# Optimization experiments

Measured on AMD Instinct MI355X. Metric: run time of the kernel, lower is better.

## Reference

```python
import jax, jax.numpy as jnp
import numpy as np

D_MODEL = 1024
NUM_HEADS = 16
HEAD_DIM = D_MODEL // NUM_HEADS


def setup_inputs() -> dict:
    key = jax.random.key(0)
    ks = jax.random.split(key, 5)
    B, S, D_IN = 2, 2048, 1024
    x = jax.random.normal(ks[0], (B, S, D_IN), dtype=jnp.float32)
    std = 0.02
    wq = jax.random.normal(ks[1], (D_MODEL, D_IN), dtype=jnp.float32) * std
    wk = jax.random.normal(ks[2], (D_MODEL, D_IN), dtype=jnp.float32) * std
    wv = jax.random.normal(ks[3], (D_MODEL, D_IN), dtype=jnp.float32) * std
    wo = jax.random.normal(ks[4], (D_IN, D_MODEL), dtype=jnp.float32) * std
    return {"x": x, "wq": wq, "wk": wk, "wv": wv, "wo": wo}


def _mha(x, wq, wk, wv, wo):
    B, S, _ = x.shape
    H, Dh = NUM_HEADS, HEAD_DIM
    # projections: Linear applies x @ W.T with W of shape [out, in]
    q = (x @ wq.T).reshape(B, S, H, Dh).transpose(0, 2, 1, 3)  # [B,H,S,Dh]
    k = (x @ wk.T).reshape(B, S, H, Dh).transpose(0, 2, 1, 3)
    v = (x @ wv.T).reshape(B, S, H, Dh).transpose(0, 2, 1, 3)
    scores = jnp.einsum('bhqd,bhkd->bhqk', q, k) / jnp.sqrt(jnp.float32(Dh))
    causal = jnp.tril(jnp.ones((S, S), dtype=bool))  # True where attended
    scores = jnp.where(causal, scores, -jnp.inf)
    attn = jax.nn.softmax(scores, axis=-1)
    out = jnp.einsum('bhqk,bhkd->bhqd', attn, v)  # [B,H,S,Dh]
    out = out.transpose(0, 2, 1, 3).reshape(B, S, H * Dh)
    return out @ wo.T


def reference(x, wq, wk, wv, wo):
    return _mha(x, wq, wk, wv, wo)
```

## Files before the change

kernel.cpp:

```cpp
#include <hip/hip_runtime.h>
#include <hip/hip_bf16.h>
#include <stdint.h>

using bf16 = __hip_bfloat16;
typedef __attribute__((ext_vector_type(4))) short shorts4;
typedef __attribute__((ext_vector_type(8))) short short8;
typedef __attribute__((ext_vector_type(4))) float floatx4;
typedef __attribute__((ext_vector_type(16))) float floatx16;
typedef __attribute__((ext_vector_type(4))) unsigned int uintx4;

constexpr int BATCH = 2;
constexpr int SEQ   = 2048;
constexpr int NH    = 16;
constexpr int DH    = 64;
constexpr int DM    = 1024;
constexpr int MROWS = BATCH * SEQ;
constexpr int OUTN  = MROWS * DM;
constexpr int WN    = DM * DM;

__device__ inline short bfbits(float x) {
    bf16 h = __float2bfloat16(x);
    return __builtin_bit_cast(short, h);
}

__device__ inline unsigned pack2(float a, float b) {
    return (unsigned)(unsigned short)bfbits(a) |
           ((unsigned)(unsigned short)bfbits(b) << 16);
}

__device__ inline void async16(bf16* lds, const bf16* g) {
    __builtin_amdgcn_global_load_lds(
        (const __attribute__((address_space(1))) unsigned int*)g,
        (__attribute__((address_space(3))) unsigned int*)lds, 16, 0, 0);
}

__device__ inline void cvt8(const float* src, bf16* dst) {
    float4 f0 = *(const float4*)(src);
    float4 f1 = *(const float4*)(src + 4);
    short8 o;
    o[0] = bfbits(f0.x); o[1] = bfbits(f0.y); o[2] = bfbits(f0.z); o[3] = bfbits(f0.w);
    o[4] = bfbits(f1.x); o[5] = bfbits(f1.y); o[6] = bfbits(f1.z); o[7] = bfbits(f1.w);
    *(short8*)(dst) = o;
}

__global__ __launch_bounds__(256)
void cvt_all(const float* __restrict__ x,  const float* __restrict__ wq,
             const float* __restrict__ wk, const float* __restrict__ wv,
             const float* __restrict__ wo, bf16* __restrict__ dst,
             bf16* __restrict__ wob)
{
    const size_t i = ((size_t)blockIdx.x * 256 + threadIdx.x) * 8;
    if (i < (size_t)OUTN + 3 * WN) {
        const float* src; size_t off;
        if (i < (size_t)OUTN)               { src = x;  off = i; }
        else if (i < (size_t)OUTN + WN)     { src = wq; off = i - OUTN; }
        else if (i < (size_t)OUTN + 2 * WN) { src = wk; off = i - OUTN - WN; }
        else                                { src = wv; off = i - OUTN - 2 * (size_t)WN; }
        cvt8(src + off, dst + i);
    } else {
        const size_t off = i - OUTN - 3 * (size_t)WN;
        cvt8(wo + off, wob + off);
    }
}

__global__ __launch_bounds__(256)
void cvt_inputs(const float* __restrict__ x,  const float* __restrict__ wq,
                const float* __restrict__ wk, const float* __restrict__ wv,
                bf16* __restrict__ dst)
{
    const size_t i = ((size_t)blockIdx.x * 256 + threadIdx.x) * 8;
    const float* src; size_t off;
    if (i < (size_t)OUTN)               { src = x;  off = i; }
    else if (i < (size_t)OUTN + WN)     { src = wq; off = i - OUTN; }
    else if (i < (size_t)OUTN + 2 * WN) { src = wk; off = i - OUTN - WN; }
    else                                { src = wv; off = i - OUTN - 2 * (size_t)WN; }
    cvt8(src + off, dst + i);
}

__global__ __launch_bounds__(256)
void cvt_wo(const float* __restrict__ wo, bf16* __restrict__ dst)
{
    const size_t i = ((size_t)blockIdx.x * 256 + threadIdx.x) * 8;
    cvt8(wo + i, dst + i);
}

template<int MODE, int NZ>
__global__ __launch_bounds__(512, 2)
void gemm_mfma(const bf16* __restrict__ A,
               const bf16* __restrict__ W0, const bf16* __restrict__ W1,
               const bf16* __restrict__ W2,
               bf16* __restrict__ C0, bf16* __restrict__ C1, bf16* __restrict__ C2,
               float* __restrict__ F)
{
    __shared__ __align__(16) bf16 smem[(1 + NZ) * 8192 * 2];

    const int t    = threadIdx.x;
    const int wave = t >> 6;
    const int lane = t & 63;
    const int quad = lane >> 4;
    const int l16  = lane & 15;
    const int m0 = blockIdx.y * 128;
    const int n0 = blockIdx.x * 128;
    const int wr = (wave >> 2) * 64;
    const int wc = (wave & 3) * 32;

    const bf16* Wp[3] = {W0, W1, W2};

    floatx4 acc[NZ][4][2] = {};

    auto stage = [&](int kt, int bb) {
        bf16* Bb = smem + bb * (1 + NZ) * 8192;
        const int k0 = kt * 64;
        #pragma unroll
        for (int p = 0; p < 2; p++) {
            const int ck = p * 512 + t;
            const int kr = ck >> 3;
            const int kg = (ck & 7) ^ (kr & 7);
            async16(Bb + ck * 8, A + (size_t)(m0 + kr) * DM + k0 + kg * 8);
            #pragma unroll
            for (int zz = 0; zz < NZ; zz++)
                async16(Bb + (1 + zz) * 8192 + ck * 8,
                        Wp[zz] + (size_t)(n0 + kr) * DM + k0 + kg * 8);
        }
    };

    stage(0, 0);
    __syncthreads();

    for (int kt = 0; kt < DM / 64; ++kt) {
        const int cur = kt & 1;
        if (kt + 1 < DM / 64) stage(kt + 1, cur ^ 1);

        const bf16* Bb = smem + cur * (1 + NZ) * 8192;

        #pragma unroll
        for (int ks = 0; ks < 2; ks++) {
            short8 af[4];
            #pragma unroll
            for (int i = 0; i < 4; i++) {
                const int r = wr + i * 16 + l16;
                af[i] = *(const short8*)(Bb + r * 64 + ((ks * 4 + quad) ^ (r & 7)) * 8);
            }
            #pragma unroll
            for (int zz = 0; zz < NZ; zz++) {
                short8 wf[2];
                #pragma unroll
                for (int j = 0; j < 2; j++) {
                    const int n = wc + j * 16 + l16;
                    wf[j] = *(const short8*)(Bb + (1 + zz) * 8192 + n * 64 +
                                             ((ks * 4 + quad) ^ (n & 7)) * 8);
                }
                __builtin_amdgcn_s_setprio(1);
                #pragma unroll
                for (int i = 0; i < 4; i++)
                    #pragma unroll
                    for (int j = 0; j < 2; j++)
                        acc[zz][i][j] = __builtin_amdgcn_mfma_f32_16x16x32_bf16(
                            af[i], wf[j], acc[zz][i][j], 0, 0, 0);
                __builtin_amdgcn_s_setprio(0);
            }
        }
        __syncthreads();
    }

    #pragma unroll
    for (int zz = 0; zz < NZ; zz++) {
        #pragma unroll
        for (int i = 0; i < 4; i++) {
            #pragma unroll
            for (int j = 0; j < 2; j++) {
                if (MODE == 0 && zz == 2) {
                    const int s0 = m0 + wr + i * 16 + quad * 4;
                    const int gn = n0 + wc + j * 16 + l16;
                    const int b = s0 >> 11, sr = s0 & (SEQ - 1);
                    const int h = gn >> 6,  d = gn & (DH - 1);
                    shorts4 pv;
                    #pragma unroll
                    for (int r = 0; r < 4; r++) pv[r] = bfbits(acc[zz][i][j][r]);
                    *(shorts4*)(C2 + (((size_t)(b * NH + h)) * DH + d) * SEQ + sr) = pv;
                } else {
                    #pragma unroll
                    for (int r = 0; r < 4; r++) {
                        const int gm = m0 + wr + i * 16 + quad * 4 + r;
                        const int gn = n0 + wc + j * 16 + l16;
                        if (MODE == 1) {
                            F[(size_t)gm * DM + gn] = acc[zz][i][j][r];
                        } else {
                            float av = acc[zz][i][j][r];
                            if (zz == 0) av *= 0.18033688f;
                            bf16* dst = (zz == 0) ? C0 : C1;
                            dst[(size_t)gm * DM + gn] = __float2bfloat16(av);
                        }
                    }
                }
            }
        }
    }
}

__global__ __launch_bounds__(512, 2)
void attn_flash(bf16* __restrict__ Q, const bf16* __restrict__ K,
                const bf16* __restrict__ Vt)
{
    __shared__ __align__(16) bf16 smem[49152];

    const int t    = threadIdx.x;
    const int wave = t >> 6;
    const int lane = t & 63;
    const int hi   = lane >> 5;
    const int l32  = lane & 31;

    const int h   = blockIdx.y;
    const int b   = blockIdx.z;
    const int qtA = blockIdx.x;
    const int qtB = 15 - qtA;
    const int hc  = h * DH;
    const size_t rowb = (size_t)b * SEQ;
    const size_t bhv  = ((size_t)(b * NH + h)) * SEQ * DH;

    const int qw    = wave & 3;
    const int khalf = wave >> 2;
    const int qrA = qtA * 128 + qw * 32;
    const int qrB = qtB * 128 + qw * 32;

    short8 qfA[4], qfB[4];
    #pragma unroll
    for (int sg = 0; sg < 4; sg++) {
        qfA[sg] = *(const short8*)(Q + (rowb + qrA + l32) * DM + hc + sg * 16 + hi * 8);
        qfB[sg] = *(const short8*)(Q + (rowb + qrB + l32) * DM + hc + sg * 16 + hi * 8);
    }

    floatx16 oaccA[2] = {}, oaccB[2] = {};
    float lsumA = 0.f, lsumB = 0.f;

    constexpr int NSLOT = 17;

    auto slotK0 = [&](int s) { return (s <= qtA ? s : s - qtA - 1) * 128; };

    auto stage = [&](int s) {
        bf16* Kb = smem + (s % 3) * 16384;
        bf16* Vb = Kb + 8192;
        const int k0 = slotK0(s);
        #pragma unroll
        for (int p = 0; p < 2; p++) {
            const int ck = p * 512 + t;
            const int kr = ck >> 3;
            const int kg = (ck & 7) ^ (kr & 7);
            async16(Kb + ck * 8, K + (rowb + k0 + kr) * DM + hc + kg * 8);
            const int vr = ck >> 4;
            const int vg = (ck & 15) ^ (vr & 15);
            async16(Vb + ck * 8, Vt + bhv + (size_t)vr * SEQ + k0 + vg * 8);
        }
    };

    auto computeStage = [&](int s, int k0, int qrow, const short8* qf,
                            floatx16* oacc, float& lsum) {
        const int kbase = k0 + khalf * 64;
        if (kbase > qrow + 31) return;
        const bf16* Ks = smem + (s % 3) * 16384;
        const bf16* Vs = Ks + 8192;
        const int qg = qrow + l32;

        #pragma unroll
        for (int kt = 0; kt < 2; kt++) {
            const int kb = kbase + kt * 32;
            if (kb > qrow + 31) continue;

            const int krow = khalf * 64 + kt * 32 + l32;
            floatx16 sc = {};
            #pragma unroll
            for (int sg = 0; sg < 4; sg++) {
                const int g = (sg * 2 + hi) ^ (krow & 7);
                short8 kf = *(const short8*)(Ks + krow * 64 + g * 8);
                sc = __builtin_amdgcn_mfma_f32_32x32x16_bf16(kf, qf[sg], sc, 0, 0, 0);
            }

            if (kb + 31 > qrow) {
                #pragma unroll
                for (int r = 0; r < 16; r++) {
                    const int key = kb + (r & 3) + 8 * (r >> 2) + 4 * hi;
                    sc[r] = (key <= qg) ? sc[r] : -1e30f;
                }
            }

            #pragma unroll
            for (int r = 0; r < 16; r++) {
                const float p = __builtin_amdgcn_exp2f(sc[r]);
                sc[r] = p;
                lsum += p;
            }

            unsigned d[4][2];
            #pragma unroll
            for (int g = 0; g < 4; g++) {
                d[g][0] = pack2(sc[4 * g + 0], sc[4 * g + 1]);
                d[g][1] = pack2(sc[4 * g + 2], sc[4 * g + 3]);
            }

            #pragma unroll
            for (int h16 = 0; h16 < 2; h16++) {
                const unsigned a0 = d[h16 * 2][0],     a1 = d[h16 * 2][1];
                const unsigned b0 = d[h16 * 2 + 1][0], b1 = d[h16 * 2 + 1][1];
                const unsigned mine0 = hi ? b0 : a0, mine1 = hi ? b1 : a1;
                const unsigned give0 = hi ? a0 : b0, give1 = hi ? a1 : b1;
                const unsigned r0 = (unsigned)__shfl_xor((int)give0, 32, 64);
                const unsigned r1 = (unsigned)__shfl_xor((int)give1, 32, 64);
                uintx4 pw;
                pw[0] = hi ? r0 : mine0;
                pw[1] = hi ? r1 : mine1;
                pw[2] = hi ? mine0 : r0;
                pw[3] = hi ? mine1 : r1;
                short8 pb = __builtin_bit_cast(short8, pw);

                const int Gbase = khalf * 8 + kt * 4 + h16 * 2 + hi;
                #pragma unroll
                for (int tile = 0; tile < 2; tile++) {
                    const int vrow = tile * 32 + l32;
                    const int vg = Gbase ^ (vrow & 15);
                    short8 vf = *(const short8*)(Vs + vrow * 128 + vg * 8);
                    oacc[tile] = __builtin_amdgcn_mfma_f32_32x32x16_bf16(vf, pb, oacc[tile], 0, 0, 0);
                }
            }
        }
    };

    stage(0);
    stage(1);
    for (int s = 0; s < NSLOT - 1; ++s) {
        asm volatile("s_waitcnt vmcnt(4)" ::: "memory");
        __builtin_amdgcn_s_barrier();
        if (s + 2 < NSLOT) stage(s + 2);
        if (s <= qtA) computeStage(s, s * 128, qrA, qfA, oaccA, lsumA);
        else          computeStage(s, (s - qtA - 1) * 128, qrB, qfB, oaccB, lsumB);
    }
    asm volatile("s_waitcnt vmcnt(0)" ::: "memory");
    __builtin_amdgcn_s_barrier();
    computeStage(NSLOT - 1, (NSLOT - 1 - qtA - 1) * 128, qrB, qfB, oaccB, lsumB);

    lsumA += __shfl_xor(lsumA, 32, 64);
    lsumB += __shfl_xor(lsumB, 32, 64);

    __syncthreads();
    float* dmp = (float*)smem;
    float* lP  = dmp + 2 * 4 * 32 * 66;
    if (khalf == 1) {
        #pragma unroll
        for (int m = 0; m < 2; m++) {
            const floatx16* oc = m ? oaccB : oaccA;
            #pragma unroll
            for (int tile = 0; tile < 2; tile++)
                #pragma unroll
                for (int r = 0; r < 16; r++) {
                    const int dd = tile * 32 + (r & 3) + 8 * (r >> 2) + 4 * hi;
                    dmp[((m * 4 + qw) * 32 + l32) * 66 + dd] = oc[tile][r];
                }
            if (!hi) lP[(m * 4 + qw) * 32 + l32] = m ? lsumB : lsumA;
        }
    }
    __syncthreads();

    if (khalf == 0) {
        bf16* T8 = smem + 34304 + qw * 2304;
        #pragma unroll
        for (int m = 0; m < 2; m++) {
            const floatx16* oc = m ? oaccB : oaccA;
            const float lt = (m ? lsumB : lsumA) + lP[(m * 4 + qw) * 32 + l32];
            const float invl = 1.0f / lt;
            const int qrow = m ? qrB : qrA;
            #pragma unroll
            for (int tile = 0; tile < 2; tile++)
                #pragma unroll
                for (int rq = 0; rq < 4; rq++) {
                    shorts4 v4;
                    #pragma unroll
                    for (int sg = 0; sg < 4; sg++) {
                        const int r = rq * 4 + sg;
                        const int dd = tile * 32 + (r & 3) + 8 * (r >> 2) + 4 * hi;
                        const float comb = oc[tile][r] + dmp[((m * 4 + qw) * 32 + l32) * 66 + dd];
                        v4[sg] = bfbits(comb * invl);
                    }
                    *(shorts4*)(T8 + l32 * 72 + tile * 32 + rq * 8 + hi * 4) = v4;
                }
            asm volatile("s_waitcnt lgkmcnt(0)" ::: "memory");
            #pragma unroll
            for (int p2 = 0; p2 < 4; p2++) {
                const int rq = (lane >> 3) + p2 * 8;
                const int dd = (lane & 7) * 8;
                short8 v8 = *(const short8*)(T8 + rq * 72 + dd);
                *(short8*)(Q + (rowb + qrow + rq) * DM + hc + dd) = v8;
            }
            asm volatile("s_waitcnt lgkmcnt(0)" ::: "memory");
        }
    }
}

extern "C" void kernel_launch(void* const* d_in, const int* in_sizes, int n_in,
                              void* d_out, int out_size, void* d_ws, size_t ws_size,
                              hipStream_t stream)
{
    const float* x  = (const float*)d_in[0];
    const float* wq = (const float*)d_in[1];
    const float* wk = (const float*)d_in[2];
    const float* wv = (const float*)d_in[3];
    const float* wo = (const float*)d_in[4];
    float* out = (float*)d_out;

    bf16* qb = (bf16*)d_ws;
    bf16* kb = qb + (size_t)OUTN;
    bf16* vb = kb + (size_t)OUTN;

    bf16* xb  = (bf16*)d_out;
    bf16* wqb = xb + (size_t)OUTN;
    bf16* wkb = wqb + WN;
    bf16* wvb = wkb + WN;

    const bool wsBig = ws_size >= (size_t)(3 * (size_t)OUTN + WN) * sizeof(bf16);

    if (wsBig) {
        bf16* wob = vb + (size_t)OUTN;
        cvt_all<<<(OUTN + 4 * WN) / (8 * 256), 256, 0, stream>>>(
            x, wq, wk, wv, wo, xb, wob);
        gemm_mfma<0, 3><<<dim3(DM / 128, MROWS / 128), dim3(512), 0, stream>>>(
            xb, wqb, wkb, wvb, qb, kb, vb, nullptr);
        attn_flash<<<dim3(8, NH, BATCH), dim3(512), 0, stream>>>(qb, kb, vb);
        gemm_mfma<1, 1><<<dim3(DM / 128, MROWS / 128), dim3(512), 0, stream>>>(
            qb, wob, nullptr, nullptr, nullptr, nullptr, nullptr, out);
    } else {
        cvt_inputs<<<(OUTN + 3 * WN) / (8 * 256), 256, 0, stream>>>(x, wq, wk, wv, xb);
        gemm_mfma<0, 3><<<dim3(DM / 128, MROWS / 128), dim3(512), 0, stream>>>(
            xb, wqb, wkb, wvb, qb, kb, vb, nullptr);
        attn_flash<<<dim3(8, NH, BATCH), dim3(512), 0, stream>>>(qb, kb, vb);
        bf16* wob = kb;
        cvt_wo<<<WN / (8 * 256), 256, 0, stream>>>(wo, wob);
        gemm_mfma<1, 1><<<dim3(DM / 128, MROWS / 128), dim3(512), 0, stream>>>(
            qb, wob, nullptr, nullptr, nullptr, nullptr, nullptr, out);
    }
}
```

Before: 159.1 us.

## Rewrite QKV GEMM with 256x256 tiles, per-projection grid z, and split prefetch

The fused QKV projection, which used 128x128 tiles with all three weights staged per block, becomes a dedicated kernel with 256x256 tiles and one projection per blockIdx.z. Its K loop is split into four MFMA phases, each fenced by barriers and sched_barrier, with the next tile's A and W halves prefetched between phases. The goal is higher arithmetic intensity per LDS byte and better overlap of global loads with MFMA work. The costs are 128 KB of shared memory per block (the launch bound still asks for 2 blocks per CU, which may not fit), more barriers, a larger accumulator register footprint, and fewer blocks in the grid. The output projection and attention body are only refactored into non-templated code.

```diff
diff --git a/kernel.cpp b/kernel.cpp
--- a/kernel.cpp
+++ b/kernel.cpp
@@ -84,15 +84,171 @@
     cvt8(wo + i, dst + i);
 }
 
-template<int MODE, int NZ>
 __global__ __launch_bounds__(512, 2)
-void gemm_mfma(const bf16* __restrict__ A,
-               const bf16* __restrict__ W0, const bf16* __restrict__ W1,
-               const bf16* __restrict__ W2,
-               bf16* __restrict__ C0, bf16* __restrict__ C1, bf16* __restrict__ C2,
+void gemm_qkv(const bf16* __restrict__ A,
+              const bf16* __restrict__ W0, const bf16* __restrict__ W1,
+              const bf16* __restrict__ W2,
+              bf16* __restrict__ C0, bf16* __restrict__ C1, bf16* __restrict__ C2)
+{
+    __shared__ __align__(16) bf16 smem[65536];
+
+    const int t    = threadIdx.x;
+    const int wave = t >> 6;
+    const int lane = t & 63;
+    const int quad = lane >> 4;
+    const int l16  = lane & 15;
+    const int n0 = blockIdx.x * 256;
+    const int m0 = blockIdx.y * 256;
+    const int z  = blockIdx.z;
+    const bf16* W = (z == 0) ? W0 : ((z == 1) ? W1 : W2);
+
+    const int wm = wave >> 2;
+    const int wn = wave & 3;
+
+    floatx4 acc[8][4] = {};
+
+    auto stageHalf = [&](int kt, int bb, int tb, int h) {
+        const bf16* src = tb ? W : A;
+        const int br = tb ? n0 : m0;
+        bf16* dst = smem + bb * 32768 + tb * 16384 + h * 8192;
+        const int k0 = kt * 64;
+        #pragma unroll
+        for (int p = 0; p < 2; p++) {
+            const int ck = p * 512 + t;
+            const int kr = h * 128 + (ck >> 3);
+            const int kc = (ck & 7) ^ (kr & 7);
+            async16(dst + ck * 8, src + (size_t)(br + kr) * DM + k0 + kc * 8);
+        }
+    };
+
+    stageHalf(0, 0, 0, 0); stageHalf(0, 0, 0, 1);
+    stageHalf(0, 0, 1, 0); stageHalf(0, 0, 1, 1);
+    asm volatile("s_waitcnt vmcnt(0)" ::: "memory");
+    __builtin_amdgcn_s_barrier();
+
+    for (int kt = 0; kt < 16; ++kt) {
+        const int cur = kt & 1;
+        const bf16* Ab = smem + cur * 32768;
+        const bf16* Wb = Ab + 16384;
+        const bool pf = (kt + 1 < 16);
+
+        short8 af[4], ag[4], wf[4];
+
+        #pragma unroll
+        for (int i = 0; i < 4; i++) {
+            const int r = wm * 128 + i * 16 + l16;
+            af[i] = *(const short8*)(Ab + r * 64 + (quad ^ (r & 7)) * 8);
+        }
+        #pragma unroll
+        for (int j = 0; j < 4; j++) {
+            const int n = wn * 64 + j * 16 + l16;
+            wf[j] = *(const short8*)(Wb + n * 64 + (quad ^ (n & 7)) * 8);
+        }
+        if (pf) { stageHalf(kt + 1, cur ^ 1, 0, 0); stageHalf(kt + 1, cur ^ 1, 0, 1); }
+        __builtin_amdgcn_s_barrier();
+        asm volatile("s_waitcnt lgkmcnt(0)" ::: "memory");
+        __builtin_amdgcn_sched_barrier(0);
+        __builtin_amdgcn_s_setprio(1);
+        #pragma unroll
+        for (int i = 0; i < 4; i++)
+            #pragma unroll
+            for (int j = 0; j < 4; j++)
+                acc[i][j] = __builtin_amdgcn_mfma_f32_16x16x32_bf16(af[i], wf[j], acc[i][j], 0, 0, 0);
+        __builtin_amdgcn_s_setprio(0);
+        __builtin_amdgcn_s_barrier();
+
+        #pragma unroll
+        for (int i = 0; i < 4; i++) {
+            const int r = wm * 128 + 64 + i * 16 + l16;
+            ag[i] = *(const short8*)(Ab + r * 64 + (quad ^ (r & 7)) * 8);
+        }
+        if (pf) { stageHalf(kt + 1, cur ^ 1, 1, 0); stageHalf(kt + 1, cur ^ 1, 1, 1); }
+        __builtin_amdgcn_s_barrier();
+        asm volatile("s_waitcnt lgkmcnt(0)" ::: "memory");
+        __builtin_amdgcn_sched_barrier(0);
+        __builtin_amdgcn_s_setprio(1);
+        #pragma unroll
+        for (int i = 0; i < 4; i++)
+            #pragma unroll
+            for (int j = 0; j < 4; j++)
+                acc[4 + i][j] = __builtin_amdgcn_mfma_f32_16x16x32_bf16(ag[i], wf[j], acc[4 + i][j], 0, 0, 0);
+        __builtin_amdgcn_s_setprio(0);
+        __builtin_amdgcn_s_barrier();
+
+        #pragma unroll
+        for (int i = 0; i < 4; i++) {
+            const int r = wm * 128 + i * 16 + l16;
+            af[i] = *(const short8*)(Ab + r * 64 + ((4 + quad) ^ (r & 7)) * 8);
+        }
+        #pragma unroll
+        for (int j = 0; j < 4; j++) {
+            const int n = wn * 64 + j * 16 + l16;
+            wf[j] = *(const short8*)(Wb + n * 64 + ((4 + quad) ^ (n & 7)) * 8);
+        }
+        __builtin_amdgcn_s_barrier();
+        asm volatile("s_waitcnt lgkmcnt(0)" ::: "memory");
+        __builtin_amdgcn_sched_barrier(0);
+        __builtin_amdgcn_s_setprio(1);
+        #pragma unroll
+        for (int i = 0; i < 4; i++)
+            #pragma unroll
+            for (int j = 0; j < 4; j++)
+                acc[i][j] = __builtin_amdgcn_mfma_f32_16x16x32_bf16(af[i], wf[j], acc[i][j], 0, 0, 0);
+        __builtin_amdgcn_s_setprio(0);
+        __builtin_amdgcn_s_barrier();
+
+        #pragma unroll
+        for (int i = 0; i < 4; i++) {
+            const int r = wm * 128 + 64 + i * 16 + l16;
+            ag[i] = *(const short8*)(Ab + r * 64 + ((4 + quad) ^ (r & 7)) * 8);
+        }
+        __builtin_amdgcn_s_barrier();
+        asm volatile("s_waitcnt lgkmcnt(0)" ::: "memory");
+        __builtin_amdgcn_sched_barrier(0);
+        __builtin_amdgcn_s_setprio(1);
+        #pragma unroll
+        for (int i = 0; i < 4; i++)
+            #pragma unroll
+            for (int j = 0; j < 4; j++)
+                acc[4 + i][j] = __builtin_amdgcn_mfma_f32_16x16x32_bf16(ag[i], wf[j], acc[4 + i][j], 0, 0, 0);
+        __builtin_amdgcn_s_setprio(0);
+        asm volatile("s_waitcnt vmcnt(0)" ::: "memory");
+        __builtin_amdgcn_s_barrier();
+    }
+
+    #pragma unroll
+    for (int mi = 0; mi < 8; mi++) {
+        #pragma unroll
+        for (int j = 0; j < 4; j++) {
+            if (z == 2) {
+                const int s0 = m0 + wm * 128 + mi * 16 + quad * 4;
+                const int gn = n0 + wn * 64 + j * 16 + l16;
+                const int b = s0 >> 11, sr = s0 & (SEQ - 1);
+                const int h = gn >> 6,  d = gn & (DH - 1);
+                shorts4 pv;
+                #pragma unroll
+                for (int r = 0; r < 4; r++) pv[r] = bfbits(acc[mi][j][r]);
+                *(shorts4*)(C2 + (((size_t)(b * NH + h)) * DH + d) * SEQ + sr) = pv;
+            } else {
+                #pragma unroll
+                for (int r = 0; r < 4; r++) {
+                    const int gm = m0 + wm * 128 + mi * 16 + quad * 4 + r;
+                    const int gn = n0 + wn * 64 + j * 16 + l16;
+                    float av = acc[mi][j][r];
+                    if (z == 0) av *= 0.18033688f;
+                    bf16* dst = (z == 0) ? C0 : C1;
+                    dst[(size_t)gm * DM + gn] = __float2bfloat16(av);
+                }
+            }
+        }
+    }
+}
+
+__global__ __launch_bounds__(512, 2)
+void gemm_proj(const bf16* __restrict__ A, const bf16* __restrict__ W0,
                float* __restrict__ F)
 {
-    __shared__ __align__(16) bf16 smem[(1 + NZ) * 8192 * 2];
+    __shared__ __align__(16) bf16 smem[2 * 8192 * 2];
 
     const int t    = threadIdx.x;
     const int wave = t >> 6;
@@ -104,12 +260,10 @@
     const int wr = (wave >> 2) * 64;
     const int wc = (wave & 3) * 32;
 
-    const bf16* Wp[3] = {W0, W1, W2};
-
-    floatx4 acc[NZ][4][2] = {};
+    floatx4 acc[4][2] = {};
 
     auto stage = [&](int kt, int bb) {
-        bf16* Bb = smem + bb * (1 + NZ) * 8192;
+        bf16* Bb = smem + bb * 16384;
         const int k0 = kt * 64;
         #pragma unroll
         for (int p = 0; p < 2; p++) {
@@ -117,10 +271,7 @@
             const int kr = ck >> 3;
             const int kg = (ck & 7) ^ (kr & 7);
             async16(Bb + ck * 8, A + (size_t)(m0 + kr) * DM + k0 + kg * 8);
-            #pragma unroll
-            for (int zz = 0; zz < NZ; zz++)
-                async16(Bb + (1 + zz) * 8192 + ck * 8,
-                        Wp[zz] + (size_t)(n0 + kr) * DM + k0 + kg * 8);
+            async16(Bb + 8192 + ck * 8, W0 + (size_t)(n0 + kr) * DM + k0 + kg * 8);
         }
     };
 
@@ -131,68 +282,111 @@
         const int cur = kt & 1;
         if (kt + 1 < DM / 64) stage(kt + 1, cur ^ 1);
 
-        const bf16* Bb = smem + cur * (1 + NZ) * 8192;
+        const bf16* Bb = smem + cur * 16384;
 
         #pragma unroll
         for (int ks = 0; ks < 2; ks++) {
-            short8 af[4];
+            short8 af[4], wf[2];
             #pragma unroll
             for (int i = 0; i < 4; i++) {
                 const int r = wr + i * 16 + l16;
                 af[i] = *(const short8*)(Bb + r * 64 + ((ks * 4 + quad) ^ (r & 7)) * 8);
             }
             #pragma unroll
-            for (int zz = 0; zz < NZ; zz++) {
-                short8 wf[2];
+            for (int j = 0; j < 2; j++) {
+                const int n = wc + j * 16 + l16;
+                wf[j] = *(const short8*)(Bb + 8192 + n * 64 + ((ks * 4 + quad) ^ (n & 7)) * 8);
+            }
+            __builtin_amdgcn_s_setprio(1);
+            #pragma unroll
+            for (int i = 0; i < 4; i++)
                 #pragma unroll
-                for (int j = 0; j < 2; j++) {
-                    const int n = wc + j * 16 + l16;
-                    wf[j] = *(const short8*)(Bb + (1 + zz) * 8192 + n * 64 +
-                                             ((ks * 4 + quad) ^ (n & 7)) * 8);
-                }
-                __builtin_amdgcn_s_setprio(1);
-                #pragma unroll
-                for (int i = 0; i < 4; i++)
-                    #pragma unroll
-                    for (int j = 0; j < 2; j++)
-                        acc[zz][i][j] = __builtin_amdgcn_mfma_f32_16x16x32_bf16(
-                            af[i], wf[j], acc[zz][i][j], 0, 0, 0);
-                __builtin_amdgcn_s_setprio(0);
-            }
+                for (int j = 0; j < 2; j++)
+                    acc[i][j] = __builtin_amdgcn_mfma_f32_16x16x32_bf16(af[i], wf[j], acc[i][j], 0, 0, 0);
+            __builtin_amdgcn_s_setprio(0);
         }
         __syncthreads();
     }
 
     #pragma unroll
-    for (int zz = 0; zz < NZ; zz++) {
-        #pragma unroll
-        for (int i = 0; i < 4; i++) {
-            #pragma unroll
-            for (int j = 0; j < 2; j++) {
-                if (MODE == 0 && zz == 2) {
-                    const int s0 = m0 + wr + i * 16 + quad * 4;
-                    const int gn = n0 + wc + j * 16 + l16;
-                    const int b = s0 >> 11, sr = s0 & (SEQ - 1);
-                    const int h = gn >> 6,  d = gn & (DH - 1);
-                    shorts4 pv;
-                    #pragma unroll
-                    for (int r = 0; r < 4; r++) pv[r] = bfbits(acc[zz][i][j][r]);
-                    *(shorts4*)(C2 + (((size_t)(b * NH + h)) * DH + d) * SEQ + sr) = pv;
-                } else {
-                    #pragma unroll
-                    for (int r = 0; r < 4; r++) {
-                        const int gm = m0 + wr + i * 16 + quad * 4 + r;
-                        const int gn = n0 + wc + j * 16 + l16;
-                        if (MODE == 1) {
-                            F[(size_t)gm * DM + gn] = acc[zz][i][j][r];
-                        } else {
-                            float av = acc[zz][i][j][r];
-                            if (zz == 0) av *= 0.18033688f;
-                            bf16* dst = (zz == 0) ? C0 : C1;
-                            dst[(size_t)gm * DM + gn] = __float2bfloat16(av);
-                        }
-                    }
-                }
+    for (int i = 0; i < 4; i++)
+        #pragma unroll
+        for (int j = 0; j < 2; j++)
+            #pragma unroll
+            for (int r = 0; r < 4; r++) {
+                const int gm = m0 + wr + i * 16 + quad * 4 + r;
+                const int gn = n0 + wc + j * 16 + l16;
+                F[(size_t)gm * DM + gn] = acc[i][j][r];
+            }
+}
+
+__device__ __forceinline__ void attn_tile(const bf16* Ks, int kbase, int qrow,
+                                          const short8 (&qf)[4],
+                                          floatx16 (&oacc)[2], float& lsum,
+                                          int khalf, int hi, int l32)
+{
+    if (kbase > qrow + 31) return;
+    const bf16* Vs = Ks + 8192;
+    const int qg = qrow + l32;
+
+    #pragma unroll
+    for (int kt = 0; kt < 2; kt++) {
+        const int kb = kbase + kt * 32;
+        if (kb > qrow + 31) continue;
+
+        const int krow = khalf * 64 + kt * 32 + l32;
+        floatx16 sc = {};
+        #pragma unroll
+        for (int sg = 0; sg < 4; sg++) {
+            const int g = (sg * 2 + hi) ^ (krow & 7);
+            short8 kf = *(const short8*)(Ks + krow * 64 + g * 8);
+            sc = __builtin_amdgcn_mfma_f32_32x32x16_bf16(kf, qf[sg], sc, 0, 0, 0);
+        }
+
+        if (kb + 31 > qrow) {
+            #pragma unroll
+            for (int r = 0; r < 16; r++) {
+                const int key = kb + (r & 3) + 8 * (r >> 2) + 4 * hi;
+                sc[r] = (key <= qg) ? sc[r] : -1e30f;
+            }
+        }
+
+        #pragma unroll
+        for (int r = 0; r < 16; r++) {
+            const float p = __builtin_amdgcn_exp2f(sc[r]);
+            sc[r] = p;
+            lsum += p;
+        }
+
+        unsigned d[4][2];
+        #pragma unroll
+        for (int g = 0; g < 4; g++) {
+            d[g][0] = pack2(sc[4 * g + 0], sc[4 * g + 1]);
+            d[g][1] = pack2(sc[4 * g + 2], sc[4 * g + 3]);
+        }
+
+        #pragma unroll
+        for (int h16 = 0; h16 < 2; h16++) {
+            const unsigned a0 = d[h16 * 2][0],     a1 = d[h16 * 2][1];
+            const unsigned b0 = d[h16 * 2 + 1][0], b1 = d[h16 * 2 + 1][1];
+            const unsigned mine0 = hi ? b0 : a0, mine1 = hi ? b1 : a1;
+            const unsigned give0 = hi ? a0 : b0, give1 = hi ? a1 : b1;
+            const unsigned r0 = (unsigned)__shfl_xor((int)give0, 32, 64);
+            const unsigned r1 = (unsigned)__shfl_xor((int)give1, 32, 64);
+            uintx4 pw;
+            pw[0] = hi ? r0 : mine0;
+            pw[1] = hi ? r1 : mine1;
+            pw[2] = hi ? mine0 : r0;
+            pw[3] = hi ? mine1 : r1;
+            short8 pb = __builtin_bit_cast(short8, pw);
+
+            const int Gbase = khalf * 8 + kt * 4 + h16 * 2 + hi;
+            #pragma unroll
+            for (int tile = 0; tile < 2; tile++) {
+                const int vrow = tile * 32 + l32;
+                const int vg = Gbase ^ (vrow & 15);
+                short8 vf = *(const short8*)(Vs + vrow * 128 + vg * 8);
+                oacc[tile] = __builtin_amdgcn_mfma_f32_32x32x16_bf16(vf, pb, oacc[tile], 0, 0, 0);
             }
         }
     }
@@ -253,89 +447,22 @@
         }
     };
 
-    auto computeStage = [&](int s, int k0, int qrow, const short8* qf,
-                            floatx16* oacc, float& lsum) {
-        const int kbase = k0 + khalf * 64;
-        if (kbase > qrow + 31) return;
-        const bf16* Ks = smem + (s % 3) * 16384;
-        const bf16* Vs = Ks + 8192;
-        const int qg = qrow + l32;
-
-        #pragma unroll
-        for (int kt = 0; kt < 2; kt++) {
-            const int kb = kbase + kt * 32;
-            if (kb > qrow + 31) continue;
-
-            const int krow = khalf * 64 + kt * 32 + l32;
-            floatx16 sc = {};
-            #pragma unroll
-            for (int sg = 0; sg < 4; sg++) {
-                const int g = (sg * 2 + hi) ^ (krow & 7);
-                short8 kf = *(const short8*)(Ks + krow * 64 + g * 8);
-                sc = __builtin_amdgcn_mfma_f32_32x32x16_bf16(kf, qf[sg], sc, 0, 0, 0);
-            }
-
-            if (kb + 31 > qrow) {
-                #pragma unroll
-                for (int r = 0; r < 16; r++) {
-                    const int key = kb + (r & 3) + 8 * (r >> 2) + 4 * hi;
-                    sc[r] = (key <= qg) ? sc[r] : -1e30f;
-                }
-            }
-
-            #pragma unroll
-            for (int r = 0; r < 16; r++) {
-                const float p = __builtin_amdgcn_exp2f(sc[r]);
-                sc[r] = p;
-                lsum += p;
-            }
-
-            unsigned d[4][2];
-            #pragma unroll
-            for (int g = 0; g < 4; g++) {
-                d[g][0] = pack2(sc[4 * g + 0], sc[4 * g + 1]);
-                d[g][1] = pack2(sc[4 * g + 2], sc[4 * g + 3]);
-            }
-
-            #pragma unroll
-            for (int h16 = 0; h16 < 2; h16++) {
-                const unsigned a0 = d[h16 * 2][0],     a1 = d[h16 * 2][1];
-                const unsigned b0 = d[h16 * 2 + 1][0], b1 = d[h16 * 2 + 1][1];
-                const unsigned mine0 = hi ? b0 : a0, mine1 = hi ? b1 : a1;
-                const unsigned give0 = hi ? a0 : b0, give1 = hi ? a1 : b1;
-                const unsigned r0 = (unsigned)__shfl_xor((int)give0, 32, 64);
-                const unsigned r1 = (unsigned)__shfl_xor((int)give1, 32, 64);
-                uintx4 pw;
-                pw[0] = hi ? r0 : mine0;
-                pw[1] = hi ? r1 : mine1;
-                pw[2] = hi ? mine0 : r0;
-                pw[3] = hi ? mine1 : r1;
-                short8 pb = __builtin_bit_cast(short8, pw);
-
-                const int Gbase = khalf * 8 + kt * 4 + h16 * 2 + hi;
-                #pragma unroll
-                for (int tile = 0; tile < 2; tile++) {
-                    const int vrow = tile * 32 + l32;
-                    const int vg = Gbase ^ (vrow & 15);
-                    short8 vf = *(const short8*)(Vs + vrow * 128 + vg * 8);
-                    oacc[tile] = __builtin_amdgcn_mfma_f32_32x32x16_bf16(vf, pb, oacc[tile], 0, 0, 0);
-                }
-            }
-        }
-    };
-
     stage(0);
     stage(1);
     for (int s = 0; s < NSLOT - 1; ++s) {
         asm volatile("s_waitcnt vmcnt(4)" ::: "memory");
         __builtin_amdgcn_s_barrier();
         if (s + 2 < NSLOT) stage(s + 2);
-        if (s <= qtA) computeStage(s, s * 128, qrA, qfA, oaccA, lsumA);
-        else          computeStage(s, (s - qtA - 1) * 128, qrB, qfB, oaccB, lsumB);
+        const bf16* Ks = smem + (s % 3) * 16384;
+        if (s <= qtA)
+            attn_tile(Ks, s * 128 + khalf * 64, qrA, qfA, oaccA, lsumA, khalf, hi, l32);
+        else
+            attn_tile(Ks, (s - qtA - 1) * 128 + khalf * 64, qrB, qfB, oaccB, lsumB, khalf, hi, l32);
     }
     asm volatile("s_waitcnt vmcnt(0)" ::: "memory");
     __builtin_amdgcn_s_barrier();
-    computeStage(NSLOT - 1, (NSLOT - 1 - qtA - 1) * 128, qrB, qfB, oaccB, lsumB);
+    attn_tile(smem + ((NSLOT - 1) % 3) * 16384,
+              (NSLOT - 2 - qtA) * 128 + khalf * 64, qrB, qfB, oaccB, lsumB, khalf, hi, l32);
 
     lsumA += __shfl_xor(lsumA, 32, 64);
     lsumB += __shfl_xor(lsumB, 32, 64);
@@ -420,19 +547,19 @@
         bf16* wob = vb + (size_t)OUTN;
         cvt_all<<<(OUTN + 4 * WN) / (8 * 256), 256, 0, stream>>>(
             x, wq, wk, wv, wo, xb, wob);
-        gemm_mfma<0, 3><<<dim3(DM / 128, MROWS / 128), dim3(512), 0, stream>>>(
-            xb, wqb, wkb, wvb, qb, kb, vb, nullptr);
+        gemm_qkv<<<dim3(DM / 256, MROWS / 256, 3), dim3(512), 0, stream>>>(
+            xb, wqb, wkb, wvb, qb, kb, vb);
         attn_flash<<<dim3(8, NH, BATCH), dim3(512), 0, stream>>>(qb, kb, vb);
-        gemm_mfma<1, 1><<<dim3(DM / 128, MROWS / 128), dim3(512), 0, stream>>>(
-            qb, wob, nullptr, nullptr, nullptr, nullptr, nullptr, out);
+        gemm_proj<<<dim3(DM / 128, MROWS / 128), dim3(512), 0, stream>>>(
+            qb, wob, out);
     } else {
         cvt_inputs<<<(OUTN + 3 * WN) / (8 * 256), 256, 0, stream>>>(x, wq, wk, wv, xb);
-        gemm_mfma<0, 3><<<dim3(DM / 128, MROWS / 128), dim3(512), 0, stream>>>(
-            xb, wqb, wkb, wvb, qb, kb, vb, nullptr);
+        gemm_qkv<<<dim3(DM / 256, MROWS / 256, 3), dim3(512), 0, stream>>>(
+            xb, wqb, wkb, wvb, qb, kb, vb);
         attn_flash<<<dim3(8, NH, BATCH), dim3(512), 0, stream>>>(qb, kb, vb);
         bf16* wob = kb;
         cvt_wo<<<WN / (8 * 256), 256, 0, stream>>>(wo, wob);
-        gemm_mfma<1, 1><<<dim3(DM / 128, MROWS / 128), dim3(512), 0, stream>>>(
-            qb, wob, nullptr, nullptr, nullptr, nullptr, nullptr, out);
-    }
-}
+        gemm_proj<<<dim3(DM / 128, MROWS / 128), dim3(512), 0, stream>>>(
+            qb, wob, out);
+    }
+}
```

New measurement: 168.0 us. 5.6% more time.
